# Kernel tuning notes

Hardware: AMD Instinct MI355X
Metric: run time of the kernel (lower is better)

The kernel has to match this reference:

```python
import jax, jax.numpy as jnp
import numpy as np

# ---- model hyperparameters (match init_kwargs) ----
N_ATOMS = 16000
N_EDGES = 256000
F = 128          # n_atom_basis
NF = 32          # n_filters
L = 3            # n_interactions
N_RBF = 20
CUTOFF = 5.0
MAX_Z = 100
INV_SQRT_F = np.float32(1.0 / np.sqrt(F))
INV_SQRT_2NF = np.float32(1.0 / np.sqrt(2 * NF))
SQ2 = np.float32(np.sqrt(2.0)); SQ3 = np.float32(np.sqrt(3.0)); SQ6 = np.float32(np.sqrt(6.0))
LOG2 = np.float32(np.log(2.0))


def ssp(x):
    # shifted softplus: softplus(x) - log(2)
    return jax.nn.softplus(x) - LOG2


def setup_inputs() -> dict:
    key = jax.random.key(0)
    k = jax.random.split(key, 16)
    Z = jax.random.randint(k[0], (N_ATOMS,), 0, MAX_Z)
    r_ij = jax.random.normal(k[1], (N_EDGES, 3), dtype=jnp.float32) * 2.0
    idx_i = jnp.sort(jax.random.randint(k[2], (N_EDGES,), 0, N_ATOMS))
    idx_j = jax.random.randint(k[3], (N_EDGES,), 0, N_ATOMS)
    # parameters (e3nn Linear: N(0,1) weights with explicit 1/sqrt(fan_in) in the math;
    # filter-network Dense: fan-in scaled weights, zero bias; padding_idx=0 -> zero row)
    emb = jax.random.normal(k[4], (MAX_Z, F), dtype=jnp.float32).at[0].set(0.0)
    W_pe = jax.random.normal(k[5], (F, F), dtype=jnp.float32)
    W0s = jax.random.normal(k[6], (L, F, NF), dtype=jnp.float32)   # in2f, 0e path
    W0v = jax.random.normal(k[7], (L, F, NF), dtype=jnp.float32)   # in2f, 1o path
    Wf1 = jax.random.normal(k[8], (L, N_RBF, NF), dtype=jnp.float32) / np.sqrt(N_RBF)
    bf1 = jnp.zeros((L, NF), jnp.float32)
    Wf2 = jax.random.normal(k[9], (L, NF, 6 * NF), dtype=jnp.float32) / np.sqrt(NF)
    bf2 = jnp.zeros((L, 6 * NF), jnp.float32)
    As = jax.random.normal(k[10], (L, 2 * NF, F), dtype=jnp.float32)  # f2out_1 0e
    Av = jax.random.normal(k[11], (L, 2 * NF, F), dtype=jnp.float32)  # f2out_1 1o
    Bs = jax.random.normal(k[12], (L, F, F), dtype=jnp.float32)       # f2out_2 0e
    Bv = jax.random.normal(k[13], (L, F, F), dtype=jnp.float32)       # f2out_2 1o
    return dict(Z=Z, r_ij=r_ij, idx_i=idx_i, idx_j=idx_j, emb=emb, W_pe=W_pe,
                W0s=W0s, W0v=W0v, Wf1=Wf1, bf1=bf1, Wf2=Wf2, bf2=bf2,
                As=As, Av=Av, Bs=Bs, Bv=Bv)


def _interaction(xs, xv, idx_i, idx_j, f_ij, rcut, Yv,
                 W0s, W0v, Wf1, bf1, Wf2, bf2, As, Av, Bs, Bv):
    n_atoms = xs.shape[0]
    # in2f: e3nn o3.Linear (per-l channel mixing, fan-in normalized)
    hs = (xs @ W0s) * INV_SQRT_F                        # [N, NF]  (0e)
    hv = jnp.einsum('nfc,fg->ngc', xv, W0v) * INV_SQRT_F  # [N, NF, 3] (1o)
    sj = hs[idx_j]                                      # gather neighbors [E, NF]
    vj = hv[idx_j]                                      # [E, NF, 3]
    # FullTensorProduct (0e+1o) x Y(0e+1o); Y0 = 1, Y1 = sqrt(3)*r_hat (component norm)
    Yb = Yv[:, None, :]                                 # [E, 1, 3]
    t0a = sj                                            # 0e x 0e -> 0e
    t0b = jnp.einsum('efc,ec->ef', vj, Yv) / SQ3        # 1o x 1o -> 0e
    t1a = sj[:, :, None] * Yb                           # 0e x 1o -> 1o
    t1b = vj                                            # 1o x 0e -> 1o
    t1e = jnp.cross(vj, Yb) / SQ2                       # 1o x 1o -> 1e
    ux, uy, uz = vj[..., 0], vj[..., 1], vj[..., 2]
    wx, wy, wz = Yv[:, None, 0], Yv[:, None, 1], Yv[:, None, 2]
    t2e = jnp.stack([(ux * wy + uy * wx) / SQ2,         # 1o x 1o -> 2e (sym traceless)
                     (uy * wz + uz * wy) / SQ2,
                     (2 * uz * wz - ux * wx - uy * wy) / SQ6,
                     (ux * wz + uz * wx) / SQ2,
                     (ux * wx - uy * wy) / SQ2], axis=-1)  # [E, NF, 5]
    # filter network + cutoff envelope: W_ij [E, 6*NF] (one scalar per irrep)
    W = (ssp(f_ij @ Wf1 + bf1) @ Wf2 + bf2) * rcut[:, None]
    w0a, w0b, w1a, w1b, w1e, w2e = jnp.split(W, 6, axis=1)
    E = sj.shape[0]
    # elementwise tensor product (scale each irrep by its scalar), then scatter-add
    y_all = jnp.concatenate([
        t0a * w0a, t0b * w0b,
        (t1a * w1a[..., None]).reshape(E, -1),
        (t1b * w1b[..., None]).reshape(E, -1),
        (t1e * w1e[..., None]).reshape(E, -1),
        (t2e * w2e[..., None]).reshape(E, -1)], axis=1)   # [E, 16*NF]
    agg = jax.ops.segment_sum(y_all, idx_i, num_segments=n_atoms)  # [N, 16*NF]
    s_in = agg[:, :2 * NF]
    v_in = agg[:, 2 * NF:8 * NF].reshape(n_atoms, 2 * NF, 3)
    # f2out_1: output irreps are F x (0e+1o) -> 1e and 2e channels have no path (dropped)
    os = ssp((s_in @ As) * INV_SQRT_2NF)                # f2out_1 + scalar activation
    ov = jnp.einsum('nfc,fg->ngc', v_in, Av) * INV_SQRT_2NF
    os = (os @ Bs) * INV_SQRT_F                         # f2out_2
    ov = jnp.einsum('nfc,fg->ngc', ov, Bv) * INV_SQRT_F
    return os, ov


def _forward(Z, r_ij, idx_i, idx_j, emb, W_pe, W0s, W0v, Wf1, bf1, Wf2, bf2, As, Av, Bs, Bv):
    xs = (emb[Z] @ W_pe) * INV_SQRT_F                   # embedding + post_embedding (0e)
    xv = jnp.zeros((xs.shape[0], F, 3), xs.dtype)       # 1o part starts at zero (no 0e->1o path)
    d = jnp.linalg.norm(r_ij, axis=1)
    offsets = jnp.linspace(0.0, CUTOFF, N_RBF).astype(jnp.float32)
    coeff = -0.5 / (offsets[1] - offsets[0]) ** 2
    f_ij = jnp.exp(coeff * (d[:, None] - offsets) ** 2)  # Gaussian RBF [E, N_RBF]
    rcut = 0.5 * (jnp.cos(np.float32(np.pi) * d / CUTOFF) + 1.0) * (d < CUTOFF)
    # spherical harmonics, normalize=True + component normalization (Y0=1, Y1=sqrt(3)*rhat);
    # the r_ij*rcut prescaling in the original doesn't change the direction, and edges with
    # rcut=0 contribute nothing since W_ij carries the rcut factor.
    Yv = SQ3 * r_ij / jnp.maximum(d, 1e-9)[:, None]
    for l in range(L):
        vs, vv = _interaction(xs, xv, idx_i, idx_j, f_ij, rcut, Yv,
                              W0s[l], W0v[l], Wf1[l], bf1[l], Wf2[l], bf2[l],
                              As[l], Av[l], Bs[l], Bv[l])
        xs = xs + vs
        xv = xv + vv
    return xs  # scalar_representation [N, F]


def reference(Z, r_ij, idx_i, idx_j, emb, W_pe, W0s, W0v, Wf1, bf1, Wf2, bf2, As, Av, Bs, Bv):
    return _forward(Z, r_ij, idx_i, idx_j, emb, W_pe, W0s, W0v, Wf1, bf1, Wf2, bf2, As, Av, Bs, Bv)
```

## Files before the change

kernel.cpp:

```cpp
#include <hip/hip_runtime.h>
#include <math.h>

constexpr int NA   = 16000;
constexpr int NE   = 256000;
constexpr int F    = 128;
constexpr int NF   = 32;
constexpr int NRBF = 20;
constexpr float CUTOFF       = 5.0f;
constexpr float INV_SQRT_F   = 0.0883883476483184f;
constexpr float INV_SQRT_2NF = 0.125f;
constexpr float INV_SQ3      = 0.5773502691896258f;
constexpr float SQ3          = 1.7320508075688772f;
constexpr float LOG2_        = 0.6931471805599453f;
constexpr float PI_          = 3.14159265358979323f;

__device__ __forceinline__ float ssp(float x) {
    return fmaxf(x, 0.0f) + __logf(1.0f + __expf(-fabsf(x))) - LOG2_;
}
__device__ __forceinline__ float rlane_f(float v, int l) {
    return __int_as_float(__builtin_amdgcn_readlane(__float_as_int(v), l));
}

__global__ void geom_kernel(const float* __restrict__ r_ij,
                            float* __restrict__ fijT,
                            float* __restrict__ yvrT) {
    int e = blockIdx.x * blockDim.x + threadIdx.x;
    if (e >= NE) return;
    float x = r_ij[3*e+0], y = r_ij[3*e+1], z = r_ij[3*e+2];
    float d = sqrtf(x*x + y*y + z*z);
    const float delta = CUTOFF / (NRBF - 1);
    const float coeff = -0.5f / (delta * delta);
    #pragma unroll
    for (int k = 0; k < NRBF; k++) {
        float t = d - delta * (float)k;
        fijT[(size_t)k*NE + e] = __expf(coeff * t * t);
    }
    float rc = 0.5f * (__cosf(PI_ * d / CUTOFF) + 1.0f);
    rc = (d < CUTOFF) ? rc : 0.0f;
    float inv = SQ3 / fmaxf(d, 1e-9f);
    yvrT[0*(size_t)NE + e] = x * inv;
    yvrT[1*(size_t)NE + e] = y * inv;
    yvrT[2*(size_t)NE + e] = z * inv;
    yvrT[3*(size_t)NE + e] = rc;
}

__global__ void prep_kernel(const float* __restrict__ Wf2, float* __restrict__ Wf2T) {
    int u = blockIdx.x * 256 + threadIdx.x;
    if (u >= 3*128*32) return;
    int l = u >> 12, rem = u & 4095, c = rem >> 5, k = rem & 31;
    Wf2T[u] = Wf2[(size_t)l*NF*192 + k*192 + c];
}

__global__ void prep2_kernel(const float* __restrict__ Av, const float* __restrict__ Bv,
                             float* __restrict__ AvBv) {
    int u = blockIdx.x * 256 + threadIdx.x;
    if (u >= 3*64*128) return;
    int l = u >> 13, rem = u & 8191, f = rem >> 7, c = rem & 127;
    const float* av = Av + (size_t)l*64*128 + f*128;
    const float* bv = Bv + (size_t)l*128*128 + c;
    float acc = 0.f;
    #pragma unroll 8
    for (int g = 0; g < 128; g++) acc += av[g] * bv[(size_t)g*128];
    AvBv[u] = acc * (INV_SQRT_2NF * INV_SQRT_F);
}

__global__ __launch_bounds__(256, 4)
void embed_kernel(const int* __restrict__ Z,
                  const float* __restrict__ emb,
                  const float* __restrict__ Wpe,
                  float* __restrict__ xs) {
    __shared__ float ER[32][128];
    __shared__ int   Zs[32];
    int t = threadIdx.x;
    int a0 = blockIdx.x * 32;
    if (t < 32) Zs[t] = Z[a0 + t];
    __syncthreads();
    {
        const float4* emb4 = (const float4*)emb;
        float4* ER4 = (float4*)&ER[0][0];
        #pragma unroll
        for (int it = 0; it < 4; it++) {
            int u4 = it*256 + t;
            int a = u4 >> 5, k4 = u4 & 31;
            ER4[u4] = emb4[(size_t)Zs[a]*32 + k4];
        }
    }
    __syncthreads();
    int c = t & 127, half = t >> 7;
    float acc[16];
    #pragma unroll
    for (int a = 0; a < 16; a++) acc[a] = 0.f;
    for (int k = 0; k < 128; k++) {
        float w = Wpe[k*128 + c];
        #pragma unroll
        for (int a = 0; a < 16; a++) acc[a] += ER[half*16 + a][k] * w;
    }
    #pragma unroll
    for (int a = 0; a < 16; a++)
        xs[(size_t)(a0 + half*16 + a)*128 + c] = acc[a] * INV_SQRT_F;
}

template <bool XV_ZERO>
__global__ __launch_bounds__(256, 4)
void h_kernel(const float* __restrict__ xs,
              const float* __restrict__ xv,
              const float* __restrict__ W0s,
              const float* __restrict__ W0v,
              float* __restrict__ hsv) {
    __shared__ float X[16][512];
    int t = threadIdx.x;
    int a0 = blockIdx.x * 16;
    {
        float* Xf = &X[0][0];
        const float4* xs4 = (const float4*)xs;
        #pragma unroll
        for (int it = 0; it < 2; it++) {
            int u4 = it*256 + t;
            int a = u4 >> 5, k4 = u4 & 31;
            *(float4*)&Xf[a*512 + k4*4] = xs4[(size_t)a0*32 + u4];
        }
        if (!XV_ZERO) {
            const float4* xv4 = (const float4*)xv;
            #pragma unroll
            for (int it = 0; it < 6; it++) {
                int u4 = it*256 + t;
                int a = u4 / 96, rem = u4 - a*96;
                *(float4*)&Xf[a*512 + 128 + rem*4] = xv4[(size_t)a0*96 + u4];
            }
        }
    }
    __syncthreads();
    int g = t & 31, r = t >> 5;
    int sel = r & 3, half = r >> 2;
    if (XV_ZERO && sel != 0) {
        #pragma unroll
        for (int a = 0; a < 8; a++) {
            int n = a0 + half*8 + a;
            hsv[(size_t)n*128 + 32 + g*3 + (sel-1)] = 0.f;
        }
        return;
    }
    const float* W = (sel == 0) ? W0s : W0v;
    int xoff = (sel == 0) ? 0 : (128 + (sel-1)*128);
    float acc[8];
    #pragma unroll
    for (int a = 0; a < 8; a++) acc[a] = 0.f;
    for (int k = 0; k < 128; k++) {
        float w = W[k*32 + g];
        #pragma unroll
        for (int a = 0; a < 8; a++) acc[a] += X[half*8 + a][xoff + k] * w;
    }
    #pragma unroll
    for (int a = 0; a < 8; a++) {
        int n = a0 + half*8 + a;
        if (sel == 0) hsv[(size_t)n*128 + g] = acc[a] * INV_SQRT_F;
        else          hsv[(size_t)n*128 + 32 + g*3 + (sel-1)] = acc[a] * INV_SQRT_F;
    }
}

template <bool DO_V>
__global__ __launch_bounds__(256, 3)
void agg_kernel(const int* __restrict__ idx_i,
                const int* __restrict__ idx_j,
                const float* __restrict__ fijT,
                const float* __restrict__ yvrT,
                const float* __restrict__ hsv,
                const float* __restrict__ Wf1,
                const float* __restrict__ bf1,
                const float* __restrict__ Wf2T,
                const float* __restrict__ bf2,
                float* __restrict__ aggG) {
    __shared__ float LWf1[NRBF*NF];
    __shared__ float HB[4][64][36];
    int t = threadIdx.x;
    for (int u = t; u < NRBF*NF; u += 256) LWf1[u] = Wf1[u];
    __syncthreads();

    int wid = t >> 6, lane = t & 63;
    int base = (blockIdx.x*4 + wid) * 64;

    int   il = idx_i[base + lane];
    int   jl = idx_j[base + lane];
    float y0l = yvrT[0*(size_t)NE + base + lane];
    float y1l = yvrT[1*(size_t)NE + base + lane];
    float y2l = yvrT[2*(size_t)NE + base + lane];
    float y3l = yvrT[3*(size_t)NE + base + lane];

    int ilp = __shfl_up(il, 1);
    unsigned long long bmask = __ballot(lane > 0 && il != ilp);

    float h[32];
    #pragma unroll
    for (int g = 0; g < 32; g++) h[g] = bf1[g];
    #pragma unroll
    for (int k = 0; k < NRBF; k++) {
        float fk = fijT[(size_t)k*NE + base + lane];
        #pragma unroll
        for (int q = 0; q < 8; q++) {
            float4 w = *(const float4*)&LWf1[k*32 + q*4];
            h[q*4+0] += fk * w.x;
            h[q*4+1] += fk * w.y;
            h[q*4+2] += fk * w.z;
            h[q*4+3] += fk * w.w;
        }
    }
    #pragma unroll
    for (int g = 0; g < 32; g++) h[g] = ssp(h[g]);
    #pragma unroll
    for (int q = 0; q < 8; q++) {
        float4 v = { h[q*4], h[q*4+1], h[q*4+2], h[q*4+3] };
        *(float4*)&HB[wid][lane][q*4] = v;
    }

    float4 w2a[8], w2b[8];
    #pragma unroll
    for (int q = 0; q < 8; q++) w2a[q] = *(const float4*)&Wf2T[lane*32 + q*4];
    if (DO_V) {
        #pragma unroll
        for (int q = 0; q < 8; q++) w2b[q] = *(const float4*)&Wf2T[(64+lane)*32 + q*4];
    }
    float bf2a = bf2[lane];
    float bf2b = DO_V ? bf2[64 + lane] : 0.f;

    int idxQ = 32 + 3*(lane - 32);

    float a0 = 0.f, a1 = 0.f, a2 = 0.f, a3 = 0.f;
    int prev = __builtin_amdgcn_readlane(il, 0);
    const float* hb = &HB[wid][0][0];

    for (int ii = 0; ii < 64; ++ii) {
        if ((bmask >> ii) & 1ull) {
            unsafeAtomicAdd(&aggG[(size_t)prev*256 + lane], a0);
            a0 = 0.f;
            if (DO_V) {
                unsafeAtomicAdd(&aggG[(size_t)prev*256 + 64 + lane],  a1);
                unsafeAtomicAdd(&aggG[(size_t)prev*256 + 128 + lane], a2);
                unsafeAtomicAdd(&aggG[(size_t)prev*256 + 192 + lane], a3);
                a1 = a2 = a3 = 0.f;
            }
            prev = __builtin_amdgcn_readlane(il, ii);
        }
        int j = __builtin_amdgcn_readlane(jl, ii);
        const float* row = hsv + (size_t)j*128;
        float q0, q1, q2;
        if (lane < 32) {
            q0 = row[lane]; q1 = q0; q2 = q0;
        } else {
            const float* p = row + idxQ;
            q0 = p[0]; q1 = p[1]; q2 = p[2];
        }
        float s0 = bf2a, s1 = bf2b;
        const float* hrow = hb + ii*36;
        #pragma unroll
        for (int qq = 0; qq < 8; qq++) {
            float4 hq = *(const float4*)&hrow[qq*4];
            s0 += hq.x*w2a[qq].x + hq.y*w2a[qq].y + hq.z*w2a[qq].z + hq.w*w2a[qq].w;
            if (DO_V)
                s1 += hq.x*w2b[qq].x + hq.y*w2b[qq].y + hq.z*w2b[qq].z + hq.w*w2b[qq].w;
        }
        float y3s = rlane_f(y3l, ii);
        float y0s = rlane_f(y0l, ii);
        float y1s = rlane_f(y1l, ii);
        float y2s = rlane_f(y2l, ii);
        float w0 = s0 * y3s;
        float dot = (q0*y0s + q1*y1s + q2*y2s) * INV_SQ3;
        float v0 = (lane < 32) ? q0 : dot;
        a0 += v0 * w0;
        if (DO_V) {
            float w1 = s1 * y3s;
            float m1 = (lane < 32) ? y0s : 1.0f;
            float m2 = (lane < 32) ? y1s : 1.0f;
            float m3 = (lane < 32) ? y2s : 1.0f;
            a1 += q0 * m1 * w1;
            a2 += q1 * m2 * w1;
            a3 += q2 * m3 * w1;
        }
    }
    unsafeAtomicAdd(&aggG[(size_t)prev*256 + lane], a0);
    if (DO_V) {
        unsafeAtomicAdd(&aggG[(size_t)prev*256 + 64 + lane],  a1);
        unsafeAtomicAdd(&aggG[(size_t)prev*256 + 128 + lane], a2);
        unsafeAtomicAdd(&aggG[(size_t)prev*256 + 192 + lane], a3);
    }
}

template <bool DO_V, bool XV_WRITE>
__global__ __launch_bounds__(256, 4)
void mlp_kernel(const float* __restrict__ aggG,
                const float* __restrict__ As,
                const float* __restrict__ Bs,
                const float* __restrict__ AvBv,
                float* __restrict__ xs,
                float* __restrict__ xv) {
    constexpr int AC = DO_V ? 256 : 64;
    __shared__ float aggL[16][AC];
    __shared__ float outL[16][128];
    int t = threadIdx.x;
    int a0 = blockIdx.x * 16;
    {
        const float4* g4 = (const float4*)(aggG + (size_t)a0*256);
        if (DO_V) {
            #pragma unroll
            for (int it = 0; it < 4; it++) {
                int u4 = it*256 + t;
                *(float4*)&aggL[0][u4*4 - (u4>>6)*(256-AC)*0] = g4[u4];
            }
        } else {
            int row = t >> 4, c4 = t & 15;
            *(float4*)&aggL[row][c4*4] = g4[row*64 + c4];
        }
    }
    __syncthreads();

    int q  = t & 31;
    int rp = t >> 5;
    const float4* As4 = (const float4*)As;
    const float4* Bs4 = (const float4*)Bs;

    {
        float ox0=0,oy0=0,oz0=0,ow0=0, ox1=0,oy1=0,oz1=0,ow1=0;
        const float4* x0p = (const float4*)&aggL[rp][0];
        const float4* x1p = (const float4*)&aggL[rp+8][0];
        #pragma unroll 4
        for (int kq = 0; kq < 16; kq++) {
            float4 x0 = x0p[kq], x1 = x1p[kq];
            float4 wa = As4[(4*kq+0)*32 + q];
            float4 wb = As4[(4*kq+1)*32 + q];
            float4 wc = As4[(4*kq+2)*32 + q];
            float4 wd = As4[(4*kq+3)*32 + q];
            ox0 += x0.x*wa.x + x0.y*wb.x + x0.z*wc.x + x0.w*wd.x;
            oy0 += x0.x*wa.y + x0.y*wb.y + x0.z*wc.y + x0.w*wd.y;
            oz0 += x0.x*wa.z + x0.y*wb.z + x0.z*wc.z + x0.w*wd.z;
            ow0 += x0.x*wa.w + x0.y*wb.w + x0.z*wc.w + x0.w*wd.w;
            ox1 += x1.x*wa.x + x1.y*wb.x + x1.z*wc.x + x1.w*wd.x;
            oy1 += x1.x*wa.y + x1.y*wb.y + x1.z*wc.y + x1.w*wd.y;
            oz1 += x1.x*wa.z + x1.y*wb.z + x1.z*wc.z + x1.w*wd.z;
            ow1 += x1.x*wa.w + x1.y*wb.w + x1.z*wc.w + x1.w*wd.w;
        }
        float4 r0 = { ssp(ox0*INV_SQRT_2NF), ssp(oy0*INV_SQRT_2NF), ssp(oz0*INV_SQRT_2NF), ssp(ow0*INV_SQRT_2NF) };
        float4 r1 = { ssp(ox1*INV_SQRT_2NF), ssp(oy1*INV_SQRT_2NF), ssp(oz1*INV_SQRT_2NF), ssp(ow1*INV_SQRT_2NF) };
        *(float4*)&outL[rp][4*q]   = r0;
        *(float4*)&outL[rp+8][4*q] = r1;
    }
    if (DO_V) {
        const float4* AB4 = (const float4*)AvBv;
        int ra[6], rc[6];
        #pragma unroll
        for (int i = 0; i < 6; i++) {
            int rv = rp + 8*i;
            ra[i] = rv/3; rc[i] = rv - 3*(rv/3);
        }
        float o[6][4];
        #pragma unroll
        for (int i = 0; i < 6; i++) { o[i][0]=0; o[i][1]=0; o[i][2]=0; o[i][3]=0; }
        const float4* vp[6];
        #pragma unroll
        for (int i = 0; i < 6; i++)
            vp[i] = (const float4*)&aggL[ra[i]][64 + rc[i]*64];
        #pragma unroll 2
        for (int kq = 0; kq < 16; kq++) {
            float4 wa = AB4[(4*kq+0)*32 + q];
            float4 wb = AB4[(4*kq+1)*32 + q];
            float4 wc = AB4[(4*kq+2)*32 + q];
            float4 wd = AB4[(4*kq+3)*32 + q];
            #pragma unroll
            for (int i = 0; i < 6; i++) {
                float4 x = vp[i][kq];
                o[i][0] += x.x*wa.x + x.y*wb.x + x.z*wc.x + x.w*wd.x;
                o[i][1] += x.x*wa.y + x.y*wb.y + x.z*wc.y + x.w*wd.y;
                o[i][2] += x.x*wa.z + x.y*wb.z + x.z*wc.z + x.w*wd.z;
                o[i][3] += x.x*wa.w + x.y*wb.w + x.z*wc.w + x.w*wd.w;
            }
        }
        #pragma unroll
        for (int i = 0; i < 6; i++) {
            float4* p = (float4*)&xv[(size_t)(a0+ra[i])*384 + rc[i]*128 + 4*q];
            if (XV_WRITE) {
                float4 c = { o[i][0], o[i][1], o[i][2], o[i][3] };
                *p = c;
            } else {
                float4 c = *p;
                c.x += o[i][0]; c.y += o[i][1]; c.z += o[i][2]; c.w += o[i][3];
                *p = c;
            }
        }
    }
    __syncthreads();
    {
        float ox0=0,oy0=0,oz0=0,ow0=0, ox1=0,oy1=0,oz1=0,ow1=0;
        const float4* x0p = (const float4*)&outL[rp][0];
        const float4* x1p = (const float4*)&outL[rp+8][0];
        #pragma unroll 4
        for (int kq = 0; kq < 32; kq++) {
            float4 x0 = x0p[kq], x1 = x1p[kq];
            float4 wa = Bs4[(4*kq+0)*32 + q];
            float4 wb = Bs4[(4*kq+1)*32 + q];
            float4 wc = Bs4[(4*kq+2)*32 + q];
            float4 wd = Bs4[(4*kq+3)*32 + q];
            ox0 += x0.x*wa.x + x0.y*wb.x + x0.z*wc.x + x0.w*wd.x;
            oy0 += x0.x*wa.y + x0.y*wb.y + x0.z*wc.y + x0.w*wd.y;
            oz0 += x0.x*wa.z + x0.y*wb.z + x0.z*wc.z + x0.w*wd.z;
            ow0 += x0.x*wa.w + x0.y*wb.w + x0.z*wc.w + x0.w*wd.w;
            ox1 += x1.x*wa.x + x1.y*wb.x + x1.z*wc.x + x1.w*wd.x;
            oy1 += x1.x*wa.y + x1.y*wb.y + x1.z*wc.y + x1.w*wd.y;
            oz1 += x1.x*wa.z + x1.y*wb.z + x1.z*wc.z + x1.w*wd.z;
            ow1 += x1.x*wa.w + x1.y*wb.w + x1.z*wc.w + x1.w*wd.w;
        }
        float4* p0 = (float4*)&xs[(size_t)(a0+rp)*128 + 4*q];
        float4* p1 = (float4*)&xs[(size_t)(a0+rp+8)*128 + 4*q];
        float4 c0 = *p0, c1 = *p1;
        c0.x += ox0*INV_SQRT_F; c0.y += oy0*INV_SQRT_F; c0.z += oz0*INV_SQRT_F; c0.w += ow0*INV_SQRT_F;
        c1.x += ox1*INV_SQRT_F; c1.y += oy1*INV_SQRT_F; c1.z += oz1*INV_SQRT_F; c1.w += ow1*INV_SQRT_F;
        *p0 = c0; *p1 = c1;
    }
}

extern "C" void kernel_launch(void* const* d_in, const int* in_sizes, int n_in,
                              void* d_out, int out_size, void* d_ws, size_t ws_size,
                              hipStream_t stream) {
    (void)in_sizes; (void)n_in; (void)out_size; (void)ws_size;
    const int*   Z     = (const int*)  d_in[0];
    const float* r_ij  = (const float*)d_in[1];
    const int*   idx_i = (const int*)  d_in[2];
    const int*   idx_j = (const int*)  d_in[3];
    const float* emb   = (const float*)d_in[4];
    const float* Wpe   = (const float*)d_in[5];
    const float* W0s   = (const float*)d_in[6];
    const float* W0v   = (const float*)d_in[7];
    const float* Wf1   = (const float*)d_in[8];
    const float* bf1   = (const float*)d_in[9];
    const float* Wf2   = (const float*)d_in[10];
    const float* bf2   = (const float*)d_in[11];
    const float* As    = (const float*)d_in[12];
    const float* Av    = (const float*)d_in[13];
    const float* Bs    = (const float*)d_in[14];
    const float* Bv    = (const float*)d_in[15];

    float* xs = (float*)d_out;
    float* ws = (float*)d_ws;
    float* fijT = ws;
    float* yvrT = fijT + (size_t)NE*NRBF;
    float* xv   = yvrT + (size_t)NE*4;
    float* hsv  = xv   + (size_t)NA*F*3;
    float* aggG = hsv  + (size_t)NA*F;
    float* Wf2T = aggG + (size_t)NA*256;
    float* AvBv = Wf2T + (size_t)3*128*32;

    geom_kernel<<<(NE+255)/256, 256, 0, stream>>>(r_ij, fijT, yvrT);
    prep_kernel<<<(3*128*32+255)/256, 256, 0, stream>>>(Wf2, Wf2T);
    prep2_kernel<<<(3*64*128+255)/256, 256, 0, stream>>>(Av, Bv, AvBv);
    embed_kernel<<<NA/32, 256, 0, stream>>>(Z, emb, Wpe, xs);

    for (int l = 0; l < 3; l++) {
        if (l == 0)
            h_kernel<true><<<NA/16, 256, 0, stream>>>(xs, xv,
                W0s + (size_t)l*F*NF, W0v + (size_t)l*F*NF, hsv);
        else
            h_kernel<false><<<NA/16, 256, 0, stream>>>(xs, xv,
                W0s + (size_t)l*F*NF, W0v + (size_t)l*F*NF, hsv);

        hipMemsetAsync(aggG, 0, (size_t)NA*256*sizeof(float), stream);

        if (l < 2)
            agg_kernel<true><<<NE/256, 256, 0, stream>>>(idx_i, idx_j, fijT, yvrT, hsv,
                Wf1 + (size_t)l*NRBF*NF, bf1 + (size_t)l*NF,
                Wf2T + (size_t)l*128*32, bf2 + (size_t)l*6*NF, aggG);
        else
            agg_kernel<false><<<NE/256, 256, 0, stream>>>(idx_i, idx_j, fijT, yvrT, hsv,
                Wf1 + (size_t)l*NRBF*NF, bf1 + (size_t)l*NF,
                Wf2T + (size_t)l*128*32, bf2 + (size_t)l*6*NF, aggG);

        if (l == 0)
            mlp_kernel<true, true><<<NA/16, 256, 0, stream>>>(aggG,
                As + (size_t)l*2*NF*F, Bs + (size_t)l*F*F, AvBv + (size_t)l*64*128, xs, xv);
        else if (l == 1)
            mlp_kernel<true, false><<<NA/16, 256, 0, stream>>>(aggG,
                As + (size_t)l*2*NF*F, Bs + (size_t)l*F*F, AvBv + (size_t)l*64*128, xs, xv);
        else
            mlp_kernel<false, false><<<NA/16, 256, 0, stream>>>(aggG,
                As + (size_t)l*2*NF*F, Bs + (size_t)l*F*F, AvBv + (size_t)l*64*128, xs, xv);
    }
}
```

Baseline: 440.4 us.

## Use packed fp16 dot2 for filter network in edge aggregation kernel

Converts the filter-network weights (Wf1, Wf2) and the per-edge RBF features and hidden activations to packed half2 and computes the two small dense layers with v_dot2 fp16->fp32 instructions. This halves the ALU ops and the LDS traffic for the per-edge filter MLP, and halves register use for the weight tiles, so launch bounds are raised from 3 to 6 waves. The cost is reduced precision in the filter weights and activations, which can add error. It also makes a cosmetic cleanup of the mlp load loop.

```diff
diff --git a/kernel.cpp b/kernel.cpp
--- a/kernel.cpp
+++ b/kernel.cpp
@@ -14,11 +14,17 @@
 constexpr float LOG2_        = 0.6931471805599453f;
 constexpr float PI_          = 3.14159265358979323f;
 
+typedef _Float16 h2 __attribute__((ext_vector_type(2)));
+
 __device__ __forceinline__ float ssp(float x) {
     return fmaxf(x, 0.0f) + __logf(1.0f + __expf(-fabsf(x))) - LOG2_;
 }
-__device__ __forceinline__ float rlane_f(float v, int l) {
-    return __int_as_float(__builtin_amdgcn_readlane(__float_as_int(v), l));
+__device__ __forceinline__ float fdot2(h2 a, h2 b, float c) {
+#if __has_builtin(__builtin_amdgcn_fdot2)
+    return __builtin_amdgcn_fdot2(a, b, c, false);
+#else
+    return c + (float)a[0]*(float)b[0] + (float)a[1]*(float)b[1];
+#endif
 }
 
 __global__ void geom_kernel(const float* __restrict__ r_ij,
@@ -44,11 +50,19 @@
     yvrT[3*(size_t)NE + e] = rc;
 }
 
-__global__ void prep_kernel(const float* __restrict__ Wf2, float* __restrict__ Wf2T) {
+__global__ void preph_kernel(const float* __restrict__ Wf2, const float* __restrict__ Wf1,
+                             h2* __restrict__ Wf2H, h2* __restrict__ Wf1H) {
     int u = blockIdx.x * 256 + threadIdx.x;
-    if (u >= 3*128*32) return;
-    int l = u >> 12, rem = u & 4095, c = rem >> 5, k = rem & 31;
-    Wf2T[u] = Wf2[(size_t)l*NF*192 + k*192 + c];
+    if (u < 3*128*16) {
+        int l = u / (128*16), rem = u % (128*16), c = rem >> 4, k2 = rem & 15;
+        const float* W = Wf2 + (size_t)l*NF*192;
+        Wf2H[u] = h2{(_Float16)W[(2*k2)*192 + c], (_Float16)W[(2*k2+1)*192 + c]};
+    }
+    if (u < 3*320) {
+        int l = u / 320, rem = u % 320, k2 = rem >> 5, g = rem & 31;
+        const float* W = Wf1 + (size_t)l*NRBF*NF;
+        Wf1H[u] = h2{(_Float16)W[(2*k2)*32 + g], (_Float16)W[(2*k2+1)*32 + g]};
+    }
 }
 
 __global__ void prep2_kernel(const float* __restrict__ Av, const float* __restrict__ Bv,
@@ -159,21 +173,21 @@
 }
 
 template <bool DO_V>
-__global__ __launch_bounds__(256, 3)
+__global__ __launch_bounds__(256, 6)
 void agg_kernel(const int* __restrict__ idx_i,
                 const int* __restrict__ idx_j,
                 const float* __restrict__ fijT,
                 const float* __restrict__ yvrT,
                 const float* __restrict__ hsv,
-                const float* __restrict__ Wf1,
+                const h2* __restrict__ Wf1H,
                 const float* __restrict__ bf1,
-                const float* __restrict__ Wf2T,
+                const h2* __restrict__ Wf2H,
                 const float* __restrict__ bf2,
                 float* __restrict__ aggG) {
-    __shared__ float LWf1[NRBF*NF];
-    __shared__ float HB[4][64][36];
+    __shared__ h2 LW1[320];
+    __shared__ h2 HB[4][64][18];
     int t = threadIdx.x;
-    for (int u = t; u < NRBF*NF; u += 256) LWf1[u] = Wf1[u];
+    for (int u = t; u < 320; u += 256) LW1[u] = Wf1H[u];
     __syncthreads();
 
     int wid = t >> 6, lane = t & 63;
@@ -189,35 +203,34 @@
     int ilp = __shfl_up(il, 1);
     unsigned long long bmask = __ballot(lane > 0 && il != ilp);
 
+    h2 fp[10];
+    #pragma unroll
+    for (int k2 = 0; k2 < 10; k2++) {
+        float fa = fijT[(size_t)(2*k2)*NE + base + lane];
+        float fb = fijT[(size_t)(2*k2+1)*NE + base + lane];
+        fp[k2] = h2{(_Float16)fa, (_Float16)fb};
+    }
     float h[32];
     #pragma unroll
     for (int g = 0; g < 32; g++) h[g] = bf1[g];
     #pragma unroll
-    for (int k = 0; k < NRBF; k++) {
-        float fk = fijT[(size_t)k*NE + base + lane];
-        #pragma unroll
-        for (int q = 0; q < 8; q++) {
-            float4 w = *(const float4*)&LWf1[k*32 + q*4];
-            h[q*4+0] += fk * w.x;
-            h[q*4+1] += fk * w.y;
-            h[q*4+2] += fk * w.z;
-            h[q*4+3] += fk * w.w;
-        }
+    for (int k2 = 0; k2 < 10; k2++) {
+        #pragma unroll
+        for (int g = 0; g < 32; g++)
+            h[g] = fdot2(fp[k2], LW1[k2*32 + g], h[g]);
     }
     #pragma unroll
     for (int g = 0; g < 32; g++) h[g] = ssp(h[g]);
     #pragma unroll
-    for (int q = 0; q < 8; q++) {
-        float4 v = { h[q*4], h[q*4+1], h[q*4+2], h[q*4+3] };
-        *(float4*)&HB[wid][lane][q*4] = v;
-    }
-
-    float4 w2a[8], w2b[8];
-    #pragma unroll
-    for (int q = 0; q < 8; q++) w2a[q] = *(const float4*)&Wf2T[lane*32 + q*4];
+    for (int i = 0; i < 16; i++)
+        HB[wid][lane][i] = h2{(_Float16)h[2*i], (_Float16)h[2*i+1]};
+
+    h2 w2a[16], w2b[16];
+    #pragma unroll
+    for (int k2 = 0; k2 < 16; k2++) w2a[k2] = Wf2H[lane*16 + k2];
     if (DO_V) {
         #pragma unroll
-        for (int q = 0; q < 8; q++) w2b[q] = *(const float4*)&Wf2T[(64+lane)*32 + q*4];
+        for (int k2 = 0; k2 < 16; k2++) w2b[k2] = Wf2H[(64+lane)*16 + k2];
     }
     float bf2a = bf2[lane];
     float bf2b = DO_V ? bf2[64 + lane] : 0.f;
@@ -226,7 +239,6 @@
 
     float a0 = 0.f, a1 = 0.f, a2 = 0.f, a3 = 0.f;
     int prev = __builtin_amdgcn_readlane(il, 0);
-    const float* hb = &HB[wid][0][0];
 
     for (int ii = 0; ii < 64; ++ii) {
         if ((bmask >> ii) & 1ull) {
@@ -250,18 +262,17 @@
             q0 = p[0]; q1 = p[1]; q2 = p[2];
         }
         float s0 = bf2a, s1 = bf2b;
-        const float* hrow = hb + ii*36;
-        #pragma unroll
-        for (int qq = 0; qq < 8; qq++) {
-            float4 hq = *(const float4*)&hrow[qq*4];
-            s0 += hq.x*w2a[qq].x + hq.y*w2a[qq].y + hq.z*w2a[qq].z + hq.w*w2a[qq].w;
-            if (DO_V)
-                s1 += hq.x*w2b[qq].x + hq.y*w2b[qq].y + hq.z*w2b[qq].z + hq.w*w2b[qq].w;
-        }
-        float y3s = rlane_f(y3l, ii);
-        float y0s = rlane_f(y0l, ii);
-        float y1s = rlane_f(y1l, ii);
-        float y2s = rlane_f(y2l, ii);
+        const h2* hrow = &HB[wid][ii][0];
+        #pragma unroll
+        for (int k2 = 0; k2 < 16; k2++) {
+            h2 hq = hrow[k2];
+            s0 = fdot2(hq, w2a[k2], s0);
+            if (DO_V) s1 = fdot2(hq, w2b[k2], s1);
+        }
+        float y3s = __int_as_float(__builtin_amdgcn_readlane(__float_as_int(y3l), ii));
+        float y0s = __int_as_float(__builtin_amdgcn_readlane(__float_as_int(y0l), ii));
+        float y1s = __int_as_float(__builtin_amdgcn_readlane(__float_as_int(y1l), ii));
+        float y2s = __int_as_float(__builtin_amdgcn_readlane(__float_as_int(y2l), ii));
         float w0 = s0 * y3s;
         float dot = (q0*y0s + q1*y1s + q2*y2s) * INV_SQ3;
         float v0 = (lane < 32) ? q0 : dot;
@@ -300,11 +311,9 @@
     {
         const float4* g4 = (const float4*)(aggG + (size_t)a0*256);
         if (DO_V) {
+            float4* l4 = (float4*)&aggL[0][0];
             #pragma unroll
-            for (int it = 0; it < 4; it++) {
-                int u4 = it*256 + t;
-                *(float4*)&aggL[0][u4*4 - (u4>>6)*(256-AC)*0] = g4[u4];
-            }
+            for (int it = 0; it < 4; it++) l4[it*256 + t] = g4[it*256 + t];
         } else {
             int row = t >> 4, c4 = t & 15;
             *(float4*)&aggL[row][c4*4] = g4[row*64 + c4];
@@ -443,11 +452,12 @@
     float* xv   = yvrT + (size_t)NE*4;
     float* hsv  = xv   + (size_t)NA*F*3;
     float* aggG = hsv  + (size_t)NA*F;
-    float* Wf2T = aggG + (size_t)NA*256;
-    float* AvBv = Wf2T + (size_t)3*128*32;
+    float* AvBv = aggG + (size_t)NA*256;
+    h2*    Wf2H = (h2*)(AvBv + (size_t)3*64*128);
+    h2*    Wf1H = Wf2H + (size_t)3*128*16;
 
     geom_kernel<<<(NE+255)/256, 256, 0, stream>>>(r_ij, fijT, yvrT);
-    prep_kernel<<<(3*128*32+255)/256, 256, 0, stream>>>(Wf2, Wf2T);
+    preph_kernel<<<24, 256, 0, stream>>>(Wf2, Wf1, Wf2H, Wf1H);
     prep2_kernel<<<(3*64*128+255)/256, 256, 0, stream>>>(Av, Bv, AvBv);
     embed_kernel<<<NA/32, 256, 0, stream>>>(Z, emb, Wpe, xs);
 
@@ -463,12 +473,12 @@
 
         if (l < 2)
             agg_kernel<true><<<NE/256, 256, 0, stream>>>(idx_i, idx_j, fijT, yvrT, hsv,
-                Wf1 + (size_t)l*NRBF*NF, bf1 + (size_t)l*NF,
-                Wf2T + (size_t)l*128*32, bf2 + (size_t)l*6*NF, aggG);
+                Wf1H + (size_t)l*320, bf1 + (size_t)l*NF,
+                Wf2H + (size_t)l*128*16, bf2 + (size_t)l*6*NF, aggG);
         else
             agg_kernel<false><<<NE/256, 256, 0, stream>>>(idx_i, idx_j, fijT, yvrT, hsv,
-                Wf1 + (size_t)l*NRBF*NF, bf1 + (size_t)l*NF,
-                Wf2T + (size_t)l*128*32, bf2 + (size_t)l*6*NF, aggG);
+                Wf1H + (size_t)l*320, bf1 + (size_t)l*NF,
+                Wf2H + (size_t)l*128*16, bf2 + (size_t)l*6*NF, aggG);
 
         if (l == 0)
             mlp_kernel<true, true><<<NA/16, 256, 0, stream>>>(aggG,
```

Measured after the change: 400.0 us. 9.2% less time.
